# Kernel tuning notes

Measured on AMD Instinct MI355X. Metric: run time of the kernel, lower is better.

Reference implementation:

```python
import jax, jax.numpy as jnp
import numpy as np

AUX_LOSS_ALPHA = 0.01
TOP_K = 2
N_EXPERTS = 64


def setup_inputs() -> dict:
    key = jax.random.key(0)
    k1, k2 = jax.random.split(key)
    B, S, H, E = 4, 4096, 2048, N_EXPERTS
    hidden_states = jax.random.normal(k1, (B, S, H), dtype=jnp.float32)
    # kaiming_uniform_(a=sqrt(5)) ~ U(-1/sqrt(H), 1/sqrt(H))
    bound = 1.0 / np.sqrt(H)
    weight = jax.random.uniform(k2, (E, H), dtype=jnp.float32, minval=-bound, maxval=bound)
    return {"hidden_states": hidden_states, "weight": weight}


def reference(hidden_states, weight):
    B, S, H = hidden_states.shape
    E, K = N_EXPERTS, TOP_K
    x = hidden_states.reshape(-1, H)              # [T, H], T = B*S
    logits = jnp.einsum('th,eh->te', x, weight)   # router GEMM [T, E]
    scores = jax.nn.softmax(logits, axis=-1)
    topk_weight, topk_idx = jax.lax.top_k(scores, K)  # [T, K]
    # norm_topk_prob (K > 1)
    topk_weight = topk_weight / (jnp.sum(topk_weight, axis=-1, keepdims=True) + 1e-20)
    # seq_aux auxiliary loss (training path)
    idx2d = topk_idx.reshape(B, S * K)            # [B, S*K]
    ce = jnp.zeros((B, E), dtype=scores.dtype)
    ce = ce.at[jnp.arange(B)[:, None], idx2d].add(1.0)
    ce = ce / (S * K / E)
    scores3 = scores.reshape(B, S, E)
    aux_loss = jnp.mean(jnp.sum(ce * jnp.mean(scores3, axis=1), axis=1)) * AUX_LOSS_ALPHA
    return topk_idx, topk_weight, aux_loss
```

## Files before the change

### kernel.cpp

```cpp
#include <hip/hip_runtime.h>
#include <math.h>


#define TT 16384
#define HH 2048
#define EE 64
#define BB 4
#define M_TOK 16
#define KCH 256
#define TAU 2e-3f
#define NREP 8
#define NBLK (TT / M_TOK)

typedef float v4f __attribute__((ext_vector_type(4)));
typedef float f4v __attribute__((ext_vector_type(4)));
typedef short s8v __attribute__((ext_vector_type(8)));

__device__ __forceinline__ unsigned short f2bf(float f) {
    unsigned u = __float_as_uint(f);
    return (unsigned short)((u + 0x7fffu + ((u >> 16) & 1u)) >> 16);
}
__device__ __forceinline__ float bf2f(unsigned short h) {
    return __uint_as_float(((unsigned)h) << 16);
}

__global__ void prep_b(const float* __restrict__ w,
                       unsigned short* __restrict__ bhi,
                       unsigned short* __restrict__ blo,
                       float* __restrict__ zreg) {
    if (blockIdx.x == 0) {
        for (int i = threadIdx.x; i < 2 * NREP * BB * EE; i += 256) zreg[i] = 0.f;
    }
    int idx = blockIdx.x * blockDim.x + threadIdx.x;
    int j    = idx & 7;
    int lane = (idx >> 3) & 63;
    int ks   = (idx >> 9) & 63;
    int nt   = idx >> 15;
    int e = nt * 16 + (lane & 15);
    int k = ks * 32 + (lane >> 4) * 8 + j;
    float f = w[e * HH + k];
    unsigned short h = f2bf(f);
    bhi[idx] = h;
    blo[idx] = f2bf(f - bf2f(h));
}

__global__ __launch_bounds__(256) void gemm_gate(
    const float* __restrict__ x,
    const unsigned short* __restrict__ bhi, const unsigned short* __restrict__ blo,
    const float* __restrict__ w,
    float* __restrict__ out_idx, float* __restrict__ out_w,
    float* __restrict__ g_cnt, float* __restrict__ g_ssum) {

    __shared__ unsigned short ahi[2][8 * 64 * 8];
    __shared__ unsigned short alo[2][8 * 64 * 8];
    __shared__ float lg[M_TOK][68];
    __shared__ float bssum[EE];
    __shared__ float bcnt[EE];
    __shared__ int   fl[M_TOK];
    __shared__ int   fl_cnt;

    const int tid  = threadIdx.x;
    const int wave = tid >> 6;
    const int lane = tid & 63;
    const int tok0 = blockIdx.x * M_TOK;
    const int m  = tid >> 4;
    const int kb = tid & 15;

    if (tid < EE) { bssum[tid] = 0.f; bcnt[tid] = 0.f; }
    if (tid == 0) fl_cnt = 0;

    v4f rx[2][4];

    auto LD = [&](int c, int s) {
        const float* __restrict__ xp = x + (size_t)(tok0 + m) * HH + c * KCH + kb * 8;
        rx[s][0] = *(const v4f*)xp;
        rx[s][1] = *(const v4f*)(xp + 4);
        rx[s][2] = *(const v4f*)(xp + 128);
        rx[s][3] = *(const v4f*)(xp + 132);
    };
    auto ST = [&](int s, int bi) {
#pragma unroll
        for (int g = 0; g < 2; ++g) {
            v4f a = rx[s][g * 2], b2 = rx[s][g * 2 + 1];
            float xs[8] = {a.x, a.y, a.z, a.w, b2.x, b2.y, b2.z, b2.w};
            s8v hv, lv;
#pragma unroll
            for (int j = 0; j < 8; ++j) {
                unsigned short h = f2bf(xs[j]);
                hv[j] = (short)h;
                lv[j] = (short)f2bf(xs[j] - bf2f(h));
            }
            const int k8i = kb + g * 16;
            const int kstep = k8i >> 2, quad = k8i & 3;
            const int entry = kstep * 64 + quad * 16 + (m ^ (quad << 1));
            *(s8v*)&ahi[bi][entry * 8] = hv;
            *(s8v*)&alo[bi][entry * 8] = lv;
        }
    };

    LD(0, 0);
    LD(1, 1);
    ST(0, 0);
    __syncthreads();

    f4v acc = {0.f, 0.f, 0.f, 0.f};
    const int rdl = lane ^ ((lane >> 4) << 1);

#pragma unroll
    for (int c = 0; c < 8; ++c) {
        const int cur = c & 1;
        if (c < 6) LD(c + 2, cur);
        if (c < 7) ST(cur ^ 1, cur ^ 1);
#pragma unroll
        for (int ks = 0; ks < 8; ++ks) {
            const int entry = ks * 64 + rdl;
            s8v af_h = *(const s8v*)&ahi[cur][entry * 8];
            s8v af_l = *(const s8v*)&alo[cur][entry * 8];
            const size_t boff = ((size_t)(wave * 64 + c * 8 + ks) * 64 + lane) * 8;
            s8v bf_h = *(const s8v*)&bhi[boff];
            s8v bf_l = *(const s8v*)&blo[boff];
            acc = __builtin_amdgcn_mfma_f32_16x16x32_bf16(af_h, bf_h, acc, 0, 0, 0);
            acc = __builtin_amdgcn_mfma_f32_16x16x32_bf16(af_h, bf_l, acc, 0, 0, 0);
            acc = __builtin_amdgcn_mfma_f32_16x16x32_bf16(af_l, bf_h, acc, 0, 0, 0);
        }
        __syncthreads();
    }

#pragma unroll
    for (int r = 0; r < 4; ++r) {
        const int row = (lane >> 4) * 4 + r;
        const int col = wave * 16 + (lane & 15);
        lg[row][col] = acc[r];
    }
    __syncthreads();

    float ssum_l = 0.f;

#pragma unroll
    for (int r = 0; r < 4; ++r) {
        const int tl = wave * 4 + r;
        const int t  = tok0 + tl;
        float l = lg[tl][lane];

        float mx = l;
#pragma unroll
        for (int off = 32; off; off >>= 1) mx = fmaxf(mx, __shfl_xor(mx, off, 64));
        float p = __expf(l - mx);
        float Z = p;
#pragma unroll
        for (int off = 32; off; off >>= 1) Z += __shfl_xor(Z, off, 64);
        ssum_l += p / Z;

        float v = l;
        int cand[3]; float cl[3];
#pragma unroll
        for (int q = 0; q < 3; ++q) {
            float bv = v; int bi = lane;
#pragma unroll
            for (int off = 32; off; off >>= 1) {
                float ov = __shfl_xor(bv, off, 64);
                int   oi = __shfl_xor(bi, off, 64);
                if (ov > bv || (ov == bv && oi < bi)) { bv = ov; bi = oi; }
            }
            cand[q] = bi; cl[q] = bv;
            if (lane == bi) v = -3.4e38f;
        }

        if (lane == 0) {
            atomicAdd(&bcnt[cand[0]], 1.f);
            atomicAdd(&bcnt[cand[1]], 1.f);
            float w1 = 1.f / (1.f + __expf(cl[1] - cl[0]));
            out_idx[t * 2]     = (float)cand[0];
            out_idx[t * 2 + 1] = (float)cand[1];
            out_w[t * 2]       = w1;
            out_w[t * 2 + 1]   = 1.f - w1;
            if (cl[0] - cl[1] < TAU || cl[1] - cl[2] < TAU) {
                int pos = atomicAdd(&fl_cnt, 1);
                fl[pos] = tl;
            }
        }
    }

    atomicAdd(&bssum[lane], ssum_l);
    __syncthreads();

    {
        const int b   = tok0 >> 12;
        const int rep = (blockIdx.x & (NREP - 1)) * (BB * EE);
        if (tid < EE)
            atomicAdd(&g_cnt[rep + b * EE + tid], bcnt[tid]);
        else if (tid < 2 * EE)
            atomicAdd(&g_ssum[rep + b * EE + (tid - EE)], bssum[tid - EE]);
    }

    const int nfl = fl_cnt;
    for (int i = wave; i < nfl; i += 4) {
        const int tl = fl[i];
        const int t  = tok0 + tl;
        float l = lg[tl][lane];

        float v = l;
        int cand4[4];
#pragma unroll
        for (int q = 0; q < 4; ++q) {
            float bv = v; int bi = lane;
#pragma unroll
            for (int off = 32; off; off >>= 1) {
                float ov = __shfl_xor(bv, off, 64);
                int   oi = __shfl_xor(bi, off, 64);
                if (ov > bv || (ov == bv && oi < bi)) { bv = ov; bi = oi; }
            }
            cand4[q] = bi;
            if (lane == bi) v = -3.4e38f;
        }

        const float* __restrict__ xt  = x + (size_t)t * HH;
        const float* __restrict__ w0p = w + (size_t)cand4[0] * HH;
        const float* __restrict__ w1p = w + (size_t)cand4[1] * HH;
        const float* __restrict__ w2p = w + (size_t)cand4[2] * HH;
        const float* __restrict__ w3p = w + (size_t)cand4[3] * HH;
        double d0 = 0.0, d1 = 0.0, d2 = 0.0, d3 = 0.0;
#pragma unroll
        for (int ii = 0; ii < 8; ++ii) {
            const int k = ii * 256 + lane * 4;
            v4f xv = *(const v4f*)(xt + k);
            v4f a0 = *(const v4f*)(w0p + k);
            v4f a1 = *(const v4f*)(w1p + k);
            v4f a2 = *(const v4f*)(w2p + k);
            v4f a3 = *(const v4f*)(w3p + k);
            double dx0 = (double)xv.x, dx1 = (double)xv.y;
            double dx2 = (double)xv.z, dx3 = (double)xv.w;
            d0 = fma(dx0, (double)a0.x, d0); d0 = fma(dx1, (double)a0.y, d0);
            d0 = fma(dx2, (double)a0.z, d0); d0 = fma(dx3, (double)a0.w, d0);
            d1 = fma(dx0, (double)a1.x, d1); d1 = fma(dx1, (double)a1.y, d1);
            d1 = fma(dx2, (double)a1.z, d1); d1 = fma(dx3, (double)a1.w, d1);
            d2 = fma(dx0, (double)a2.x, d2); d2 = fma(dx1, (double)a2.y, d2);
            d2 = fma(dx2, (double)a2.z, d2); d2 = fma(dx3, (double)a2.w, d2);
            d3 = fma(dx0, (double)a3.x, d3); d3 = fma(dx1, (double)a3.y, d3);
            d3 = fma(dx2, (double)a3.z, d3); d3 = fma(dx3, (double)a3.w, d3);
        }
#pragma unroll
        for (int off = 32; off; off >>= 1) {
            d0 += __shfl_xor(d0, off, 64);
            d1 += __shfl_xor(d1, off, 64);
            d2 += __shfl_xor(d2, off, 64);
            d3 += __shfl_xor(d3, off, 64);
        }

        double bd[4] = {d0, d1, d2, d3};
        int e1 = cand4[0]; double l1 = bd[0];
#pragma unroll
        for (int q = 1; q < 4; ++q)
            if (bd[q] > l1 || (bd[q] == l1 && cand4[q] < e1)) { l1 = bd[q]; e1 = cand4[q]; }
        int e2 = -1; double l2 = -1e300;
#pragma unroll
        for (int q = 0; q < 4; ++q) {
            if (cand4[q] == e1) continue;
            if (e2 < 0 || bd[q] > l2 || (bd[q] == l2 && cand4[q] < e2)) { l2 = bd[q]; e2 = cand4[q]; }
        }

        double w1d = 1.0 / (1.0 + exp(l2 - l1));
        if (lane == 0) {
            out_idx[t * 2]     = (float)e1;
            out_idx[t * 2 + 1] = (float)e2;
            out_w[t * 2]       = (float)w1d;
            out_w[t * 2 + 1]   = (float)(1.0 - w1d);
        }
    }
}

__global__ void finalize(const float* __restrict__ g_cnt,
                         const float* __restrict__ g_ssum,
                         float* __restrict__ aux_out) {
    int lane = threadIdx.x;
    float a = 0.f;
    for (int b = 0; b < BB; ++b) {
        float c = 0.f, ss = 0.f;
#pragma unroll
        for (int r = 0; r < NREP; ++r) {
            c  += g_cnt[r * (BB * EE) + b * EE + lane];
            ss += g_ssum[r * (BB * EE) + b * EE + lane];
        }
        a += c * ss;
    }
#pragma unroll
    for (int off = 32; off; off >>= 1) a += __shfl_xor(a, off, 64);
    if (lane == 0) aux_out[0] = a * (0.01f / (4.f * 128.f * 4096.f));
}

extern "C" void kernel_launch(void* const* d_in, const int* in_sizes, int n_in,
                              void* d_out, int out_size, void* d_ws, size_t ws_size,
                              hipStream_t stream) {
    const float* x = (const float*)d_in[0];
    const float* w = (const float*)d_in[1];
    float* out = (float*)d_out;
    float* out_idx = out;
    float* out_w   = out + 2 * TT;
    float* aux     = out + 4 * TT;

    unsigned short* bhi = (unsigned short*)d_ws;
    unsigned short* blo = bhi + (size_t)EE * HH;
    float* g_cnt  = (float*)(blo + (size_t)EE * HH);
    float* g_ssum = g_cnt + NREP * BB * EE;

    prep_b<<<(EE * HH) / 256, 256, 0, stream>>>(w, bhi, blo, g_cnt);
    gemm_gate<<<NBLK, 256, 0, stream>>>(x, bhi, blo, w, out_idx, out_w,
                                        g_cnt, g_ssum);
    finalize<<<1, 64, 0, stream>>>(g_cnt, g_ssum, aux);
}
```

Baseline: 219.6 us.

## Split router GEMM over K across waves and drop the LDS staging of A

Each wave now owns a 512-wide K slice and computes all 64 experts, instead of owning 16 experts over the full K. Each lane loads its x values straight from global memory into registers and converts them to bf16 hi/lo, so the double-buffered LDS tile and the per-chunk barriers go away. The four partial accumulators are then summed through a small LDS buffer by wave 0. Launch bounds now request 4 blocks per CU. The trade-offs are more accumulator registers, the loss of explicit software prefetch, and an extra cross-wave reduction step.

```diff
diff --git a/kernel.cpp b/kernel.cpp
--- a/kernel.cpp
+++ b/kernel.cpp
@@ -7,7 +7,6 @@
 #define EE 64
 #define BB 4
 #define M_TOK 16
-#define KCH 256
 #define TAU 2e-3f
 #define NREP 8
 #define NBLK (TT / M_TOK)
@@ -44,15 +43,14 @@
     blo[idx] = f2bf(f - bf2f(h));
 }
 
-__global__ __launch_bounds__(256) void gemm_gate(
+__global__ __launch_bounds__(256, 4) void gemm_gate(
     const float* __restrict__ x,
     const unsigned short* __restrict__ bhi, const unsigned short* __restrict__ blo,
     const float* __restrict__ w,
     float* __restrict__ out_idx, float* __restrict__ out_w,
     float* __restrict__ g_cnt, float* __restrict__ g_ssum) {
 
-    __shared__ unsigned short ahi[2][8 * 64 * 8];
-    __shared__ unsigned short alo[2][8 * 64 * 8];
+    __shared__ float accLDS[3][16][64];
     __shared__ float lg[M_TOK][68];
     __shared__ float bssum[EE];
     __shared__ float bcnt[EE];
@@ -63,74 +61,62 @@
     const int wave = tid >> 6;
     const int lane = tid & 63;
     const int tok0 = blockIdx.x * M_TOK;
-    const int m  = tid >> 4;
-    const int kb = tid & 15;
 
     if (tid < EE) { bssum[tid] = 0.f; bcnt[tid] = 0.f; }
     if (tid == 0) fl_cnt = 0;
 
-    v4f rx[2][4];
-
-    auto LD = [&](int c, int s) {
-        const float* __restrict__ xp = x + (size_t)(tok0 + m) * HH + c * KCH + kb * 8;
-        rx[s][0] = *(const v4f*)xp;
-        rx[s][1] = *(const v4f*)(xp + 4);
-        rx[s][2] = *(const v4f*)(xp + 128);
-        rx[s][3] = *(const v4f*)(xp + 132);
-    };
-    auto ST = [&](int s, int bi) {
-#pragma unroll
-        for (int g = 0; g < 2; ++g) {
-            v4f a = rx[s][g * 2], b2 = rx[s][g * 2 + 1];
-            float xs[8] = {a.x, a.y, a.z, a.w, b2.x, b2.y, b2.z, b2.w};
-            s8v hv, lv;
-#pragma unroll
-            for (int j = 0; j < 8; ++j) {
-                unsigned short h = f2bf(xs[j]);
-                hv[j] = (short)h;
-                lv[j] = (short)f2bf(xs[j] - bf2f(h));
-            }
-            const int k8i = kb + g * 16;
-            const int kstep = k8i >> 2, quad = k8i & 3;
-            const int entry = kstep * 64 + quad * 16 + (m ^ (quad << 1));
-            *(s8v*)&ahi[bi][entry * 8] = hv;
-            *(s8v*)&alo[bi][entry * 8] = lv;
-        }
-    };
-
-    LD(0, 0);
-    LD(1, 1);
-    ST(0, 0);
+    const float* __restrict__ xp =
+        x + (size_t)(tok0 + (lane & 15)) * HH + wave * 512 + (lane >> 4) * 8;
+    const unsigned short* __restrict__ bhp = bhi + ((size_t)(wave * 16) * 64 + lane) * 8;
+    const unsigned short* __restrict__ blp = blo + ((size_t)(wave * 16) * 64 + lane) * 8;
+
+    f4v acc[4];
+#pragma unroll
+    for (int nt = 0; nt < 4; ++nt) acc[nt] = f4v{0.f, 0.f, 0.f, 0.f};
+
+#pragma unroll
+    for (int ks = 0; ks < 16; ++ks) {
+        v4f xa = *(const v4f*)(xp + ks * 32);
+        v4f xb = *(const v4f*)(xp + ks * 32 + 4);
+        s8v bhv[4], blv[4];
+#pragma unroll
+        for (int nt = 0; nt < 4; ++nt) {
+            bhv[nt] = *(const s8v*)(bhp + (size_t)nt * 32768 + ks * 512);
+            blv[nt] = *(const s8v*)(blp + (size_t)nt * 32768 + ks * 512);
+        }
+        s8v ah, al;
+#pragma unroll
+        for (int j = 0; j < 8; ++j) {
+            float f = (j < 4) ? xa[j] : xb[j - 4];
+            unsigned short h = f2bf(f);
+            ah[j] = (short)h;
+            al[j] = (short)f2bf(f - bf2f(h));
+        }
+#pragma unroll
+        for (int nt = 0; nt < 4; ++nt) {
+            acc[nt] = __builtin_amdgcn_mfma_f32_16x16x32_bf16(ah, bhv[nt], acc[nt], 0, 0, 0);
+            acc[nt] = __builtin_amdgcn_mfma_f32_16x16x32_bf16(ah, blv[nt], acc[nt], 0, 0, 0);
+            acc[nt] = __builtin_amdgcn_mfma_f32_16x16x32_bf16(al, bhv[nt], acc[nt], 0, 0, 0);
+        }
+    }
+
+    if (wave != 0) {
+#pragma unroll
+        for (int nt = 0; nt < 4; ++nt)
+#pragma unroll
+            for (int r = 0; r < 4; ++r)
+                accLDS[wave - 1][nt * 4 + r][lane] = acc[nt][r];
+    }
     __syncthreads();
-
-    f4v acc = {0.f, 0.f, 0.f, 0.f};
-    const int rdl = lane ^ ((lane >> 4) << 1);
-
-#pragma unroll
-    for (int c = 0; c < 8; ++c) {
-        const int cur = c & 1;
-        if (c < 6) LD(c + 2, cur);
-        if (c < 7) ST(cur ^ 1, cur ^ 1);
-#pragma unroll
-        for (int ks = 0; ks < 8; ++ks) {
-            const int entry = ks * 64 + rdl;
-            s8v af_h = *(const s8v*)&ahi[cur][entry * 8];
-            s8v af_l = *(const s8v*)&alo[cur][entry * 8];
-            const size_t boff = ((size_t)(wave * 64 + c * 8 + ks) * 64 + lane) * 8;
-            s8v bf_h = *(const s8v*)&bhi[boff];
-            s8v bf_l = *(const s8v*)&blo[boff];
-            acc = __builtin_amdgcn_mfma_f32_16x16x32_bf16(af_h, bf_h, acc, 0, 0, 0);
-            acc = __builtin_amdgcn_mfma_f32_16x16x32_bf16(af_h, bf_l, acc, 0, 0, 0);
-            acc = __builtin_amdgcn_mfma_f32_16x16x32_bf16(af_l, bf_h, acc, 0, 0, 0);
-        }
-        __syncthreads();
-    }
-
-#pragma unroll
-    for (int r = 0; r < 4; ++r) {
-        const int row = (lane >> 4) * 4 + r;
-        const int col = wave * 16 + (lane & 15);
-        lg[row][col] = acc[r];
+    if (wave == 0) {
+#pragma unroll
+        for (int nt = 0; nt < 4; ++nt)
+#pragma unroll
+            for (int r = 0; r < 4; ++r) {
+                float s = acc[nt][r] + accLDS[0][nt * 4 + r][lane]
+                        + accLDS[1][nt * 4 + r][lane] + accLDS[2][nt * 4 + r][lane];
+                lg[(lane >> 4) * 4 + r][nt * 16 + (lane & 15)] = s;
+            }
     }
     __syncthreads();
 
```

Result: slower. 230.8 us (+5.1%).
